# Optimization experiments

Measured on AMD Instinct MI355X. Metric: run time of the kernel, lower is better.

Reference implementation:

```python
import jax, jax.numpy as jnp
import numpy as np

MAX_DET = 100
IOU_THR = 0.5


def _iou_matrix(b):
    # b: [N,4] xyxy -> [N,N] pairwise IoU
    area = jnp.clip(b[:, 2] - b[:, 0], 0) * jnp.clip(b[:, 3] - b[:, 1], 0)
    lt = jnp.maximum(b[:, None, :2], b[None, :, :2])
    rb = jnp.minimum(b[:, None, 2:], b[None, :, 2:])
    wh = jnp.clip(rb - lt, 0)
    inter = wh[..., 0] * wh[..., 1]
    union = area[:, None] + area[None, :] - inter
    return inter / jnp.maximum(union, 1e-8)


def _batched_nms(boxes, scores, classes, iou_thr, max_out):
    # torchvision batched_nms semantics: offset boxes by class id so
    # boxes of different classes never overlap, then greedy NMS.
    n = boxes.shape[0]
    order = jnp.argsort(-scores)
    b = boxes[order]
    c = classes[order]
    off = c.astype(b.dtype) * (jnp.max(b) + 1.0)
    iou = _iou_matrix(b + off[:, None])  # [N,N]

    def body(valid, _):
        idx = jnp.argmax(valid)          # highest-score surviving candidate
        any_valid = jnp.any(valid)
        new_valid = valid & ~(iou[idx] > iou_thr)
        new_valid = new_valid.at[idx].set(False)
        sel = jnp.where(any_valid, order[idx], -1)
        return new_valid, sel

    _, sel = jax.lax.scan(body, jnp.ones(n, dtype=bool), None, length=max_out)
    return sel  # [max_out] indices into original order, -1 padded


def _detect_one(cls_o, box_o, idx, cls_ids, scale, size, anchor_boxes):
    a = anchor_boxes[idx]  # [N,4] yxyx
    yc_a = (a[:, 0] + a[:, 2]) * 0.5
    xc_a = (a[:, 1] + a[:, 3]) * 0.5
    ha = a[:, 2] - a[:, 0]
    wa = a[:, 3] - a[:, 1]
    box = box_o.astype(jnp.float32)
    ty, tx, th, tw = box[:, 0], box[:, 1], box[:, 2], box[:, 3]
    w = jnp.exp(tw) * wa
    h = jnp.exp(th) * ha
    yc = ty * ha + yc_a
    xc = tx * wa + xc_a
    boxes = jnp.stack([xc - w * 0.5, yc - h * 0.5, xc + w * 0.5, yc + h * 0.5], axis=1)
    # clip_boxes_xyxy with size = img_size / img_scale
    sz = jnp.concatenate([size, size]) / scale  # [4]
    boxes = jnp.minimum(jnp.clip(boxes, 0), sz[None, :])
    scores = jax.nn.sigmoid(cls_o[:, 0]).astype(jnp.float32)
    sel = _batched_nms(boxes, scores, cls_ids, IOU_THR, MAX_DET)
    safe = jnp.maximum(sel, 0)
    valid = (sel >= 0).astype(jnp.float32)[:, None]
    det = jnp.concatenate([
        boxes[safe] * scale,
        scores[safe][:, None],
        (cls_ids[safe] + 1).astype(jnp.float32)[:, None],
    ], axis=1)
    return det * valid  # zero-pad rows past num_det


def setup_inputs() -> dict:
    key = jax.random.key(0)
    ks = jax.random.split(key, 7)
    B, N, A, C = 8, 4096, 49104, 90
    cls_outputs = jax.random.normal(ks[0], (B, N, 1), jnp.float32)
    box_outputs = jax.random.normal(ks[1], (B, N, 4), jnp.float32) * 0.2
    indices = jax.random.randint(ks[2], (B, N), 0, A)
    classes = jax.random.randint(ks[3], (B, N), 0, C)
    # anchor boxes in yxyx, roughly covering a 512x512 image
    ctr = jax.random.uniform(ks[4], (A, 2), jnp.float32, 0.0, 512.0)
    hw = jax.random.uniform(ks[5], (A, 2), jnp.float32, 16.0, 128.0)
    anchor_boxes = jnp.concatenate([ctr - hw * 0.5, ctr + hw * 0.5], axis=1)
    img_scale = jax.random.uniform(ks[6], (B,), jnp.float32, 0.5, 1.5)
    img_size = jnp.full((B, 2), 512.0, jnp.float32)
    return dict(cls_outputs=cls_outputs, box_outputs=box_outputs,
                indices=indices, classes=classes, anchor_boxes=anchor_boxes,
                img_scale=img_scale, img_size=img_size)


def reference(cls_outputs, box_outputs, indices, classes, anchor_boxes, img_scale, img_size):
    f = jax.vmap(_detect_one, in_axes=(0, 0, 0, 0, 0, 0, None))
    return f(cls_outputs, box_outputs, indices, classes, img_scale, img_size, anchor_boxes)
```

## Files before the change

### kernel.cpp

```cpp
#include <hip/hip_runtime.h>
#include <stdint.h>

#define N_DET    4096
#define HALF     2048
#define MAX_DET  100
#define NTHREADS 1024
#define SORT_THREADS 512
#define IOU_THR  0.5f

typedef unsigned long long u64;

__device__ __forceinline__ float fadd(float a, float b) { return __fadd_rn(a, b); }
__device__ __forceinline__ float fsub(float a, float b) { return __fsub_rn(a, b); }
__device__ __forceinline__ float fmul(float a, float b) { return __fmul_rn(a, b); }

struct Box { float x1, y1, x2, y2; };

__device__ __forceinline__ Box decode_box_v(const float4 bo, const float4 a,
                                            float sz0, float sz1)
{
    float yc_a = fmul(fadd(a.x, a.z), 0.5f);
    float xc_a = fmul(fadd(a.y, a.w), 0.5f);
    float ha = fsub(a.z, a.x);
    float wa = fsub(a.w, a.y);
    float ty = bo.x, tx = bo.y, th = bo.z, tw = bo.w;
    float we = fmul(expf(tw), wa);
    float he = fmul(expf(th), ha);
    float yc = fadd(fmul(ty, ha), yc_a);
    float xc = fadd(fmul(tx, wa), xc_a);
    Box r;
    r.x1 = fsub(xc, fmul(we, 0.5f));
    r.y1 = fsub(yc, fmul(he, 0.5f));
    r.x2 = fadd(xc, fmul(we, 0.5f));
    r.y2 = fadd(yc, fmul(he, 0.5f));
    r.x1 = fminf(fmaxf(r.x1, 0.f), sz0);
    r.y1 = fminf(fmaxf(r.y1, 0.f), sz1);
    r.x2 = fminf(fmaxf(r.x2, 0.f), sz0);
    r.y2 = fminf(fmaxf(r.y2, 0.f), sz1);
    return r;
}

__device__ __forceinline__ float sigmoidf_ref(float x)
{
    return __fdiv_rn(1.0f, __fadd_rn(1.0f, expf(-x)));
}

__device__ __forceinline__ bool iou_suppress(float hx1, float hy1, float hx2, float hy2, float har,
                                             float cx1, float cy1, float cx2, float cy2, float car)
{
    float lt0 = fmaxf(hx1, cx1);
    float lt1 = fmaxf(hy1, cy1);
    float rb0 = fminf(hx2, cx2);
    float rb1 = fminf(hy2, cy2);
    float w0 = fmaxf(fsub(rb0, lt0), 0.f);
    float w1 = fmaxf(fsub(rb1, lt1), 0.f);
    float inter = fmul(w0, w1);
    float uni = fsub(fadd(har, car), inter);
    float iou = __fdiv_rn(inter, fmaxf(uni, 1e-8f));
    return iou > IOU_THR;
}

__device__ __forceinline__ u64 shfl_xor_u64(u64 x, int mask)
{
    unsigned lo = (unsigned)x, hi = (unsigned)(x >> 32);
    lo = __shfl_xor(lo, mask, 64);
    hi = __shfl_xor(hi, mask, 64);
    return ((u64)hi << 32) | lo;
}

__device__ __forceinline__ void cex(u64& a, u64& b, bool desc)
{
    bool sw = desc ? (a < b) : (a > b);
    u64 ta = a, tb = b;
    a = sw ? tb : ta;
    b = sw ? ta : tb;
}

__device__ __forceinline__ void shuf_pass(u64 e[4], int d, bool desc, int l)
{
    bool lower = ((l & d) == 0);
    bool keepmax = (desc == lower);
    #pragma unroll
    for (int s = 0; s < 4; ++s) {
        u64 p = shfl_xor_u64(e[s], d);
        u64 mx = (e[s] > p) ? e[s] : p;
        u64 mn = (e[s] < p) ? e[s] : p;
        e[s] = keepmax ? mx : mn;
    }
}

__device__ __forceinline__ void shuf_pass2(u64 e[2], int d, int l)
{
    bool keepmax = ((l & d) == 0);
    #pragma unroll
    for (int s = 0; s < 2; ++s) {
        u64 p = shfl_xor_u64(e[s], d);
        u64 mx = (e[s] > p) ? e[s] : p;
        u64 mn = (e[s] < p) ? e[s] : p;
        e[s] = keepmax ? mx : mn;
    }
}

__global__ __launch_bounds__(SORT_THREADS, 1)
void dec_sort_kernel(const float* __restrict__ cls_outputs,
                     const float* __restrict__ box_outputs,
                     const int*   __restrict__ indices,
                     const float* __restrict__ anchors,
                     const float* __restrict__ img_scale,
                     const float* __restrict__ img_size,
                     float*       __restrict__ wmax,
                     u64*         __restrict__ wkeys,
                     float4*      __restrict__ wboxes)
{
    __shared__ u64   keys[HALF];
    __shared__ float wred[8];

    const int blk  = blockIdx.x;
    const int b    = blk >> 1;
    const int base = (blk & 1) * HALF;
    const int t    = threadIdx.x;
    const int l    = t & 63;

    const float* cls_b = cls_outputs + (size_t)b * N_DET;
    const float* box_b = box_outputs + (size_t)b * N_DET * 4;
    const int*   idx_b = indices + (size_t)b * N_DET;
    const float  scale = img_scale[b];
    const float  sz0   = __fdiv_rn(img_size[b * 2 + 0], scale);
    const float  sz1   = __fdiv_rn(img_size[b * 2 + 1], scale);

    u64 e[4];
    float lmax = 0.0f;
    const int4   idx4 = ((const int4*)(idx_b + base))[t];
    const float4 cl4  = ((const float4*)(cls_b + base))[t];
    const int   idxs[4] = { idx4.x, idx4.y, idx4.z, idx4.w };
    const float cls4[4] = { cl4.x, cl4.y, cl4.z, cl4.w };
    #pragma unroll
    for (int s = 0; s < 4; ++s) {
        int i = base + 4 * t + s;
        float4 bo = ((const float4*)box_b)[i];
        float4 an = ((const float4*)anchors)[idxs[s]];
        Box r = decode_box_v(bo, an, sz0, sz1);
        wboxes[(size_t)b * N_DET + i] = make_float4(r.x1, r.y1, r.x2, r.y2);
        lmax = fmaxf(lmax, fmaxf(fmaxf(r.x1, r.y1), fmaxf(r.x2, r.y2)));
        float sc = sigmoidf_ref(cls4[s]);
        e[s] = ((u64)__float_as_uint(sc) << 32) | (unsigned)(N_DET - 1 - i);
    }
    for (int o = 32; o; o >>= 1) lmax = fmaxf(lmax, __shfl_xor(lmax, o, 64));
    if (l == 0) wred[t >> 6] = lmax;

    cex(e[0], e[1], true);
    cex(e[2], e[3], false);
    for (int k = 4; k <= 128; k <<= 1) {
        bool desc = (l & (k >> 2)) == 0;
        for (int j = k >> 1; j >= 4; j >>= 1) shuf_pass(e, j >> 2, desc, l);
        cex(e[0], e[2], desc); cex(e[1], e[3], desc);
        cex(e[0], e[1], desc); cex(e[2], e[3], desc);
    }
    {
        bool desc = ((t >> 6) & 1) == 0;
        for (int j = 128; j >= 4; j >>= 1) shuf_pass(e, j >> 2, desc, l);
        cex(e[0], e[2], desc); cex(e[1], e[3], desc);
        cex(e[0], e[1], desc); cex(e[2], e[3], desc);
    }
    #pragma unroll
    for (int s = 0; s < 4; ++s) keys[4 * t + s] = e[s];

    for (int k = 512; k <= HALF; k <<= 1) {
        for (int j = k >> 1; j >= 256; j >>= 1) {
            __syncthreads();
            #pragma unroll
            for (int vv = 0; vv < 2; ++vv) {
                int v = t + vv * SORT_THREADS;
                int i   = ((v & ~(j - 1)) << 1) | (v & (j - 1));
                int ixj = i | j;
                bool desc = ((i & k) == 0);
                u64 a = keys[i], c = keys[ixj];
                bool sw = desc ? (a < c) : (a > c);
                if (sw) { keys[i] = c; keys[ixj] = a; }
            }
        }
        __syncthreads();
        u64 f[4];
        #pragma unroll
        for (int s = 0; s < 4; ++s) f[s] = keys[4 * t + s];
        bool desc = (t & (k >> 2)) == 0;
        for (int j = 128; j >= 4; j >>= 1) shuf_pass(f, j >> 2, desc, l);
        cex(f[0], f[2], desc); cex(f[1], f[3], desc);
        cex(f[0], f[1], desc); cex(f[2], f[3], desc);
        #pragma unroll
        for (int s = 0; s < 4; ++s) keys[4 * t + s] = f[s];
    }
    __syncthreads();
    u64* gk = wkeys + (size_t)b * N_DET + base;
    #pragma unroll
    for (int s = 0; s < 4; ++s) gk[4 * t + s] = keys[4 * t + s];

    if (t == 0) {
        float m = wred[0];
        #pragma unroll
        for (int k = 1; k < 8; ++k) m = fmaxf(m, wred[k]);
        wmax[blk] = m;
    }
}

__global__ __launch_bounds__(NTHREADS, 1)
void scan_kernel(const int*    __restrict__ classes,
                 const float*  __restrict__ img_scale,
                 const float*  __restrict__ wmax,
                 const u64*    __restrict__ wkeys,
                 const float4* __restrict__ wboxes,
                 float*        __restrict__ out)
{
    __shared__ u64    mstream[1024];
    __shared__ int    waveA[8];
    __shared__ float4 bbox[64];
    __shared__ float  barr[64];
    __shared__ int    borig[64];
    __shared__ u64    bkey[64];
    __shared__ u64    extp[16];
    __shared__ unsigned Cplo[16][64];
    __shared__ unsigned Cphi[16][64];
    __shared__ int    sel[MAX_DET];
    __shared__ float  selsc[MAX_DET];
    __shared__ float4 hbox4[MAX_DET];
    __shared__ float  harr[MAX_DET];
    __shared__ int    sh_count;

    const int b = blockIdx.x;
    const int t = threadIdx.x;
    const int l = t & 63;

    const int*    cls_id_b = classes + (size_t)b * N_DET;
    const float   scale    = img_scale[b];
    const u64*    gA = wkeys + (size_t)b * N_DET;
    const u64*    gB = gA + HALF;
    const float4* wb = wboxes + (size_t)b * N_DET;

    const float M = fadd(fmaxf(wmax[b * 2 + 0], wmax[b * 2 + 1]), 1.0f);

    if (t < 512) mstream[t] = gA[t];
    else         mstream[t] = gB[511 - (t - 512)];
    if (t < MAX_DET) sel[t] = -1;
    if (t == 0) sh_count = 0;
    __syncthreads();

    {
        if (t < 512) {
            u64 a = mstream[t], c = mstream[t + 512];
            if (a < c) { mstream[t] = c; mstream[t + 512] = a; }
        }
        __syncthreads();
        if (t < 512) {
            int i   = ((t & ~255) << 1) | (t & 255);
            int ixj = i | 256;
            u64 a = mstream[i], c = mstream[ixj];
            if (a < c) { mstream[i] = c; mstream[ixj] = a; }
        }
        __syncthreads();
        if (t < 256) {
            u64 f[4];
            #pragma unroll
            for (int s = 0; s < 4; ++s) f[s] = mstream[4 * t + s];
            for (int j = 128; j >= 4; j >>= 1) shuf_pass(f, j >> 2, true, l);
            cex(f[0], f[2], true); cex(f[1], f[3], true);
            cex(f[0], f[1], true); cex(f[2], f[3], true);
            #pragma unroll
            for (int s = 0; s < 4; ++s) mstream[4 * t + s] = f[s];
        }
        __syncthreads();
    }

    {
        bool isA = false;
        if (t < 512) {
            int orig = N_DET - 1 - (int)(unsigned)(mstream[t] & 0xFFFFFFFFull);
            isA = (orig < HALF);
        }
        u64 bal = __ballot(isA ? 1 : 0);
        if ((t & 63) == 0 && (t >> 6) < 8) waveA[t >> 6] = __popcll(bal);
        __syncthreads();
    }
    int pa = 0;
    #pragma unroll
    for (int w = 0; w < 8; ++w) pa += waveA[w];
    int pb = 512 - pa;

    const int j = t & 63;
    const int g = t >> 6;

    for (int c = 0; c < N_DET; c += 64) {
        int count = sh_count;
        if (count >= MAX_DET) break;

        if (c + 64 <= 512) {
            if (t < 64) {
                u64 key = mstream[c + t];
                int orig = N_DET - 1 - (int)(unsigned)(key & 0xFFFFFFFFull);
                bkey[t] = key; borig[t] = orig;
                float4 bb = wb[orig];
                float off = fmul((float)cls_id_b[orig], M);
                float x1 = fadd(bb.x, off), y1 = fadd(bb.y, off);
                float x2 = fadd(bb.z, off), y2 = fadd(bb.w, off);
                bbox[t] = make_float4(x1, y1, x2, y2);
                barr[t] = fmul(fmaxf(fsub(x2, x1), 0.f), fmaxf(fsub(y2, y1), 0.f));
            }
        } else {
            if (t < 64) {
                u64 ee[2];
                if (l < 32) {
                    int p0 = pa + 2 * l;
                    ee[0] = (p0     < HALF) ? gA[p0]     : 0ull;
                    ee[1] = (p0 + 1 < HALF) ? gA[p0 + 1] : 0ull;
                } else {
                    int p  = 2 * (l - 32);
                    int q0 = pb + 63 - p;
                    ee[0] = (q0     < HALF) ? gB[q0]     : 0ull;
                    ee[1] = (q0 - 1 < HALF && q0 - 1 >= 0) ? gB[q0 - 1] : 0ull;
                }
                shuf_pass2(ee, 32, l); shuf_pass2(ee, 16, l); shuf_pass2(ee, 8, l);
                shuf_pass2(ee, 4, l);  shuf_pass2(ee, 2, l);  shuf_pass2(ee, 1, l);
                cex(ee[0], ee[1], true);

                int orig0 = N_DET - 1 - (int)(unsigned)(ee[0] & 0xFFFFFFFFull);
                int orig1 = N_DET - 1 - (int)(unsigned)(ee[1] & 0xFFFFFFFFull);
                bool r0 = (l < 32) && (ee[0] != 0ull);
                bool r1 = (l < 32) && (ee[1] != 0ull);
                if (l < 32) {
                    #pragma unroll
                    for (int s = 0; s < 2; ++s) {
                        int  r    = 2 * l + s;
                        u64  key  = s ? ee[1] : ee[0];
                        int  orig = s ? orig1 : orig0;
                        bool ok   = s ? r1 : r0;
                        bkey[r] = key;
                        if (ok) {
                            float4 bb = wb[orig];
                            float off = fmul((float)cls_id_b[orig], M);
                            float x1 = fadd(bb.x, off), y1 = fadd(bb.y, off);
                            float x2 = fadd(bb.z, off), y2 = fadd(bb.w, off);
                            bbox[r] = make_float4(x1, y1, x2, y2);
                            barr[r] = fmul(fmaxf(fsub(x2, x1), 0.f), fmaxf(fsub(y2, y1), 0.f));
                            borig[r] = orig;
                        } else {
                            bbox[r] = make_float4(0.f, 0.f, 0.f, 0.f);
                            barr[r] = 0.f;
                            borig[r] = -1;
                        }
                    }
                }
                u64 bR0 = __ballot(r0), bR1 = __ballot(r1);
                u64 bA0 = __ballot(r0 && (orig0 < HALF));
                u64 bA1 = __ballot(r1 && (orig1 < HALF));
                int real = __popcll(bR0) + __popcll(bR1);
                int aw   = __popcll(bA0) + __popcll(bA1);
                pa += aw;
                pb += real - aw;
            }
        }
        __syncthreads();

        float4 c4  = bbox[j];
        float  car = barr[j];
        const bool valid = (borig[j] >= 0);

        bool sup = !valid;
        for (int k = g; k < count; k += 16) {
            float4 h4 = hbox4[k];
            sup = sup | iou_suppress(h4.x, h4.y, h4.z, h4.w, harr[k],
                                     c4.x, c4.y, c4.z, c4.w, car);
        }
        u64 bal = __ballot(sup ? 1 : 0);
        if ((t & 63) == 0) extp[g] = bal;

        unsigned cplo = 0, cphi = 0;
        for (int r = g + 1; r < 64; r += 16) {
            int q = j ^ r;
            float4 q4 = bbox[q];
            float qar = barr[q];
            bool hit = (q > j) & valid & (borig[q] >= 0) &
                       iou_suppress(c4.x, c4.y, c4.z, c4.w, car,
                                    q4.x, q4.y, q4.z, q4.w, qar);
            unsigned bit = hit ? 1u : 0u;
            if (q < 32) cplo |= bit << q; else cphi |= bit << (q - 32);
        }
        Cplo[g][j] = cplo;
        Cphi[g][j] = cphi;
        __syncthreads();

        if (t < 64) {
            const int lane = t;
            u64 ext = 0;
            #pragma unroll
            for (int gg = 0; gg < 16; ++gg) ext |= extp[gg];
            unsigned lo = 0, hi = 0;
            #pragma unroll
            for (int gg = 0; gg < 16; ++gg) { lo |= Cplo[gg][lane]; hi |= Cphi[gg][lane]; }
            u64 C = ((u64)hi << 32) | lo;
            u64 hasC = __ballot(C != 0ull);

            u64 alive = ~ext;
            u64 selmask = 0;
            int total = count;
            while (alive && total < MAX_DET) {
                int k = __ffsll(alive) - 1;
                selmask |= (1ull << k);
                alive &= ~(1ull << k);
                ++total;
                if ((hasC >> k) & 1ull) {
                    unsigned clo = __shfl((int)(unsigned)C, k, 64);
                    unsigned chi = __shfl((int)(unsigned)(C >> 32), k, 64);
                    alive &= ~(((u64)chi << 32) | clo);
                }
            }

            if ((selmask >> lane) & 1ull) {
                int p = count + __popcll(selmask & ((1ull << lane) - 1ull));
                hbox4[p] = bbox[lane];
                harr[p]  = barr[lane];
                sel[p]   = borig[lane];
                selsc[p] = __uint_as_float((unsigned)(bkey[lane] >> 32));
            }
            if (lane == 0) sh_count = total;
        }
        __syncthreads();
    }

    if (t >= 64) return;
    for (int r = t; r < MAX_DET; r += 64) {
        int sidx = sel[r];
        float* o = out + (size_t)b * MAX_DET * 6 + (size_t)r * 6;
        if (sidx < 0) {
            o[0] = 0.f; o[1] = 0.f; o[2] = 0.f; o[3] = 0.f; o[4] = 0.f; o[5] = 0.f;
        } else {
            float4 bb = wb[sidx];
            int c = cls_id_b[sidx];
            o[0] = fmul(bb.x, scale);
            o[1] = fmul(bb.y, scale);
            o[2] = fmul(bb.z, scale);
            o[3] = fmul(bb.w, scale);
            o[4] = selsc[r];
            o[5] = (float)(c + 1);
        }
    }
}

extern "C" void kernel_launch(void* const* d_in, const int* in_sizes, int n_in,
                              void* d_out, int out_size, void* d_ws, size_t ws_size,
                              hipStream_t stream)
{
    const float* cls_outputs = (const float*)d_in[0];
    const float* box_outputs = (const float*)d_in[1];
    const int*   indices     = (const int*)d_in[2];
    const int*   classes     = (const int*)d_in[3];
    const float* anchors     = (const float*)d_in[4];
    const float* img_scale   = (const float*)d_in[5];
    const float* img_size    = (const float*)d_in[6];
    float*       out         = (float*)d_out;

    const int B = in_sizes[5];

    char* wsb = (char*)d_ws;
    float*  wmax   = (float*)wsb;
    u64*    wkeys  = (u64*)(wsb + 1024);
    float4* wboxes = (float4*)(wsb + 1024 + (size_t)B * N_DET * sizeof(u64));

    dec_sort_kernel<<<dim3(B * 2), dim3(SORT_THREADS), 0, stream>>>(
        cls_outputs, box_outputs, indices, anchors, img_scale, img_size,
        wmax, wkeys, wboxes);

    scan_kernel<<<dim3(B), dim3(NTHREADS), 0, stream>>>(
        classes, img_scale, wmax, wkeys, wboxes, out);
}
```

Measured before the change: 37.47 us.

## Double-buffer candidate chunks and prefetch next chunk during greedy selection

Candidate chunk buffers become double-buffered. While wave 0 runs the serial greedy selection on the current chunk, wave 1 loads, merges and offsets the next chunk's boxes into the other buffer. This drops one block-wide barrier per chunk and hides the global gather latency. The merge-pointer count is now computed lazily by wave 1. The initial bitonic stages also skip sorting the discarded lower half of the merged stream, which adds some shared-state complexity.

```diff
diff --git a/kernel.cpp b/kernel.cpp
--- a/kernel.cpp
+++ b/kernel.cpp
@@ -212,11 +212,10 @@
                  float*        __restrict__ out)
 {
     __shared__ u64    mstream[1024];
-    __shared__ int    waveA[8];
-    __shared__ float4 bbox[64];
-    __shared__ float  barr[64];
-    __shared__ int    borig[64];
-    __shared__ u64    bkey[64];
+    __shared__ float4 bbox2[2][64];
+    __shared__ float  barr2[2][64];
+    __shared__ int    borig2[2][64];
+    __shared__ u64    bkey2[2][64];
     __shared__ u64    extp[16];
     __shared__ unsigned Cplo[16][64];
     __shared__ unsigned Cphi[16][64];
@@ -225,6 +224,7 @@
     __shared__ float4 hbox4[MAX_DET];
     __shared__ float  harr[MAX_DET];
     __shared__ int    sh_count;
+    __shared__ int    sh_pa, sh_pb, sh_pinit;
 
     const int b = blockIdx.x;
     const int t = threadIdx.x;
@@ -241,7 +241,7 @@
     if (t < 512) mstream[t] = gA[t];
     else         mstream[t] = gB[511 - (t - 512)];
     if (t < MAX_DET) sel[t] = -1;
-    if (t == 0) sh_count = 0;
+    if (t == 0) { sh_count = 0; sh_pinit = 0; }
     __syncthreads();
 
     {
@@ -250,14 +250,14 @@
             if (a < c) { mstream[t] = c; mstream[t + 512] = a; }
         }
         __syncthreads();
-        if (t < 512) {
+        if (t < 256) {
             int i   = ((t & ~255) << 1) | (t & 255);
             int ixj = i | 256;
             u64 a = mstream[i], c = mstream[ixj];
             if (a < c) { mstream[i] = c; mstream[ixj] = a; }
         }
         __syncthreads();
-        if (t < 256) {
+        if (t < 128) {
             u64 f[4];
             #pragma unroll
             for (int s = 0; s < 4; ++s) f[s] = mstream[4 * t + s];
@@ -270,98 +270,30 @@
         __syncthreads();
     }
 
-    {
-        bool isA = false;
-        if (t < 512) {
-            int orig = N_DET - 1 - (int)(unsigned)(mstream[t] & 0xFFFFFFFFull);
-            isA = (orig < HALF);
-        }
-        u64 bal = __ballot(isA ? 1 : 0);
-        if ((t & 63) == 0 && (t >> 6) < 8) waveA[t >> 6] = __popcll(bal);
-        __syncthreads();
-    }
-    int pa = 0;
-    #pragma unroll
-    for (int w = 0; w < 8; ++w) pa += waveA[w];
-    int pb = 512 - pa;
+    if (t < 64) {
+        u64 key = mstream[t];
+        int orig = N_DET - 1 - (int)(unsigned)(key & 0xFFFFFFFFull);
+        bkey2[0][t] = key; borig2[0][t] = orig;
+        float4 bb = wb[orig];
+        float off = fmul((float)cls_id_b[orig], M);
+        float x1 = fadd(bb.x, off), y1 = fadd(bb.y, off);
+        float x2 = fadd(bb.z, off), y2 = fadd(bb.w, off);
+        bbox2[0][t] = make_float4(x1, y1, x2, y2);
+        barr2[0][t] = fmul(fmaxf(fsub(x2, x1), 0.f), fmaxf(fsub(y2, y1), 0.f));
+    }
+    __syncthreads();
 
     const int j = t & 63;
     const int g = t >> 6;
+    int cur = 0;
 
     for (int c = 0; c < N_DET; c += 64) {
         int count = sh_count;
         if (count >= MAX_DET) break;
 
-        if (c + 64 <= 512) {
-            if (t < 64) {
-                u64 key = mstream[c + t];
-                int orig = N_DET - 1 - (int)(unsigned)(key & 0xFFFFFFFFull);
-                bkey[t] = key; borig[t] = orig;
-                float4 bb = wb[orig];
-                float off = fmul((float)cls_id_b[orig], M);
-                float x1 = fadd(bb.x, off), y1 = fadd(bb.y, off);
-                float x2 = fadd(bb.z, off), y2 = fadd(bb.w, off);
-                bbox[t] = make_float4(x1, y1, x2, y2);
-                barr[t] = fmul(fmaxf(fsub(x2, x1), 0.f), fmaxf(fsub(y2, y1), 0.f));
-            }
-        } else {
-            if (t < 64) {
-                u64 ee[2];
-                if (l < 32) {
-                    int p0 = pa + 2 * l;
-                    ee[0] = (p0     < HALF) ? gA[p0]     : 0ull;
-                    ee[1] = (p0 + 1 < HALF) ? gA[p0 + 1] : 0ull;
-                } else {
-                    int p  = 2 * (l - 32);
-                    int q0 = pb + 63 - p;
-                    ee[0] = (q0     < HALF) ? gB[q0]     : 0ull;
-                    ee[1] = (q0 - 1 < HALF && q0 - 1 >= 0) ? gB[q0 - 1] : 0ull;
-                }
-                shuf_pass2(ee, 32, l); shuf_pass2(ee, 16, l); shuf_pass2(ee, 8, l);
-                shuf_pass2(ee, 4, l);  shuf_pass2(ee, 2, l);  shuf_pass2(ee, 1, l);
-                cex(ee[0], ee[1], true);
-
-                int orig0 = N_DET - 1 - (int)(unsigned)(ee[0] & 0xFFFFFFFFull);
-                int orig1 = N_DET - 1 - (int)(unsigned)(ee[1] & 0xFFFFFFFFull);
-                bool r0 = (l < 32) && (ee[0] != 0ull);
-                bool r1 = (l < 32) && (ee[1] != 0ull);
-                if (l < 32) {
-                    #pragma unroll
-                    for (int s = 0; s < 2; ++s) {
-                        int  r    = 2 * l + s;
-                        u64  key  = s ? ee[1] : ee[0];
-                        int  orig = s ? orig1 : orig0;
-                        bool ok   = s ? r1 : r0;
-                        bkey[r] = key;
-                        if (ok) {
-                            float4 bb = wb[orig];
-                            float off = fmul((float)cls_id_b[orig], M);
-                            float x1 = fadd(bb.x, off), y1 = fadd(bb.y, off);
-                            float x2 = fadd(bb.z, off), y2 = fadd(bb.w, off);
-                            bbox[r] = make_float4(x1, y1, x2, y2);
-                            barr[r] = fmul(fmaxf(fsub(x2, x1), 0.f), fmaxf(fsub(y2, y1), 0.f));
-                            borig[r] = orig;
-                        } else {
-                            bbox[r] = make_float4(0.f, 0.f, 0.f, 0.f);
-                            barr[r] = 0.f;
-                            borig[r] = -1;
-                        }
-                    }
-                }
-                u64 bR0 = __ballot(r0), bR1 = __ballot(r1);
-                u64 bA0 = __ballot(r0 && (orig0 < HALF));
-                u64 bA1 = __ballot(r1 && (orig1 < HALF));
-                int real = __popcll(bR0) + __popcll(bR1);
-                int aw   = __popcll(bA0) + __popcll(bA1);
-                pa += aw;
-                pb += real - aw;
-            }
-        }
-        __syncthreads();
-
-        float4 c4  = bbox[j];
-        float  car = barr[j];
-        const bool valid = (borig[j] >= 0);
+        float4 c4  = bbox2[cur][j];
+        float  car = barr2[cur][j];
+        const bool valid = (borig2[cur][j] >= 0);
 
         bool sup = !valid;
         for (int k = g; k < count; k += 16) {
@@ -375,9 +307,9 @@
         unsigned cplo = 0, cphi = 0;
         for (int r = g + 1; r < 64; r += 16) {
             int q = j ^ r;
-            float4 q4 = bbox[q];
-            float qar = barr[q];
-            bool hit = (q > j) & valid & (borig[q] >= 0) &
+            float4 q4 = bbox2[cur][q];
+            float qar = barr2[cur][q];
+            bool hit = (q > j) & valid & (borig2[cur][q] >= 0) &
                        iou_suppress(c4.x, c4.y, c4.z, c4.w, car,
                                     q4.x, q4.y, q4.z, q4.w, qar);
             unsigned bit = hit ? 1u : 0u;
@@ -415,14 +347,91 @@
 
             if ((selmask >> lane) & 1ull) {
                 int p = count + __popcll(selmask & ((1ull << lane) - 1ull));
-                hbox4[p] = bbox[lane];
-                harr[p]  = barr[lane];
-                sel[p]   = borig[lane];
-                selsc[p] = __uint_as_float((unsigned)(bkey[lane] >> 32));
+                hbox4[p] = bbox2[cur][lane];
+                harr[p]  = barr2[cur][lane];
+                sel[p]   = borig2[cur][lane];
+                selsc[p] = __uint_as_float((unsigned)(bkey2[cur][lane] >> 32));
             }
             if (lane == 0) sh_count = total;
-        }
-        __syncthreads();
+        } else if (t < 128) {
+            const int cn = c + 64;
+            const int nb = cur ^ 1;
+            if (cn < N_DET) {
+                if (cn + 64 <= 512) {
+                    u64 key = mstream[cn + l];
+                    int orig = N_DET - 1 - (int)(unsigned)(key & 0xFFFFFFFFull);
+                    bkey2[nb][l] = key; borig2[nb][l] = orig;
+                    float4 bb = wb[orig];
+                    float off = fmul((float)cls_id_b[orig], M);
+                    float x1 = fadd(bb.x, off), y1 = fadd(bb.y, off);
+                    float x2 = fadd(bb.z, off), y2 = fadd(bb.w, off);
+                    bbox2[nb][l] = make_float4(x1, y1, x2, y2);
+                    barr2[nb][l] = fmul(fmaxf(fsub(x2, x1), 0.f), fmaxf(fsub(y2, y1), 0.f));
+                } else {
+                    if (sh_pinit == 0) {
+                        int cnt = 0;
+                        for (int i = l; i < 512; i += 64) {
+                            int orig = N_DET - 1 - (int)(unsigned)(mstream[i] & 0xFFFFFFFFull);
+                            cnt += (orig < HALF) ? 1 : 0;
+                        }
+                        for (int o = 32; o; o >>= 1) cnt += __shfl_xor(cnt, o, 64);
+                        if (l == 0) { sh_pa = cnt; sh_pb = 512 - cnt; sh_pinit = 1; }
+                    }
+                    int pa = sh_pa, pb = sh_pb;
+                    u64 ee[2];
+                    if (l < 32) {
+                        int p0 = pa + 2 * l;
+                        ee[0] = (p0     < HALF) ? gA[p0]     : 0ull;
+                        ee[1] = (p0 + 1 < HALF) ? gA[p0 + 1] : 0ull;
+                    } else {
+                        int p  = 2 * (l - 32);
+                        int q0 = pb + 63 - p;
+                        ee[0] = (q0     < HALF) ? gB[q0]     : 0ull;
+                        ee[1] = (q0 - 1 < HALF && q0 - 1 >= 0) ? gB[q0 - 1] : 0ull;
+                    }
+                    shuf_pass2(ee, 32, l); shuf_pass2(ee, 16, l); shuf_pass2(ee, 8, l);
+                    shuf_pass2(ee, 4, l);  shuf_pass2(ee, 2, l);  shuf_pass2(ee, 1, l);
+                    cex(ee[0], ee[1], true);
+
+                    int orig0 = N_DET - 1 - (int)(unsigned)(ee[0] & 0xFFFFFFFFull);
+                    int orig1 = N_DET - 1 - (int)(unsigned)(ee[1] & 0xFFFFFFFFull);
+                    bool r0 = (l < 32) && (ee[0] != 0ull);
+                    bool r1 = (l < 32) && (ee[1] != 0ull);
+                    if (l < 32) {
+                        #pragma unroll
+                        for (int s = 0; s < 2; ++s) {
+                            int  r    = 2 * l + s;
+                            u64  key  = s ? ee[1] : ee[0];
+                            int  orig = s ? orig1 : orig0;
+                            bool ok   = s ? r1 : r0;
+                            bkey2[nb][r] = key;
+                            if (ok) {
+                                float4 bb = wb[orig];
+                                float off = fmul((float)cls_id_b[orig], M);
+                                float x1 = fadd(bb.x, off), y1 = fadd(bb.y, off);
+                                float x2 = fadd(bb.z, off), y2 = fadd(bb.w, off);
+                                bbox2[nb][r] = make_float4(x1, y1, x2, y2);
+                                barr2[nb][r] = fmul(fmaxf(fsub(x2, x1), 0.f),
+                                                    fmaxf(fsub(y2, y1), 0.f));
+                                borig2[nb][r] = orig;
+                            } else {
+                                bbox2[nb][r] = make_float4(0.f, 0.f, 0.f, 0.f);
+                                barr2[nb][r] = 0.f;
+                                borig2[nb][r] = -1;
+                            }
+                        }
+                    }
+                    u64 bR0 = __ballot(r0), bR1 = __ballot(r1);
+                    u64 bA0 = __ballot(r0 && (orig0 < HALF));
+                    u64 bA1 = __ballot(r1 && (orig1 < HALF));
+                    int real = __popcll(bR0) + __popcll(bR1);
+                    int aw   = __popcll(bA0) + __popcll(bA1);
+                    if (l == 0) { sh_pa = pa + aw; sh_pb = pb + (real - aw); }
+                }
+            }
+        }
+        __syncthreads();
+        cur ^= 1;
     }
 
     if (t >= 64) return;
```

After: 37.16 us. Within noise of the previous version (-0.8%).
